# Kernel optimization log

Measured on AMD Instinct MI355X. Metric: run time of the kernel, lower is better.

## Reference

```python
import jax, jax.numpy as jnp
import numpy as np

B, Q, K = 4, 512, 512
QUERY_SIZE = 512
KEY_SIZE = 512
NUM_HIDDENS = 256


def setup_inputs() -> dict:
    key = jax.random.key(0)
    k1, k2, k3, k4, k5 = jax.random.split(key, 5)
    queries = jax.random.normal(k1, (B, Q, 1, QUERY_SIZE), dtype=jnp.float32)
    keys = jax.random.normal(k2, (B, 1, K, KEY_SIZE), dtype=jnp.float32)
    # nn.Linear weights (bias=False); stored as (in, out) for einsum clarity
    W_q = jax.random.normal(k3, (QUERY_SIZE, NUM_HIDDENS), dtype=jnp.float32) * (1.0 / np.sqrt(QUERY_SIZE))
    W_k = jax.random.normal(k4, (KEY_SIZE, NUM_HIDDENS), dtype=jnp.float32) * (1.0 / np.sqrt(KEY_SIZE))
    w_v = jax.random.normal(k5, (NUM_HIDDENS,), dtype=jnp.float32) * (1.0 / np.sqrt(NUM_HIDDENS))
    return {"queries": queries, "keys": keys, "W_q": W_q, "W_k": W_k, "w_v": w_v}


def reference(queries, keys, W_q, W_k, w_v):
    # Project: queries (B,Q,1,Dq) -> (B,Q,1,H); keys (B,1,K,Dk) -> (B,1,K,H)
    q = jnp.einsum('bqod,dh->bqoh', queries, W_q)
    k = jnp.einsum('bokd,dh->bokh', keys, W_k)
    # Broadcast add -> (B,Q,K,H), tanh, reduce hidden via w_v -> (B,Q,K)
    features = jnp.tanh(q + k)
    scores = jnp.einsum('bqkh,h->bqk', features, w_v)
    return scores
```

## Files before the change

kernel.cpp:

```cpp
#include <hip/hip_runtime.h>
#include <hip/hip_bf16.h>

#define HH 256
#define DD 512
#define MM 2048
#define CSCALE 2.8853900817779268f

typedef __bf16 bf16x8 __attribute__((ext_vector_type(8)));
typedef float floatx4 __attribute__((ext_vector_type(4)));

__global__ __launch_bounds__(256) void prep_kernel(
    const float* __restrict__ Wq, const float* __restrict__ Wk,
    const float* __restrict__ wv,
    const float* __restrict__ queries, const float* __restrict__ keys,
    __bf16* __restrict__ Wt, __bf16* __restrict__ Xbf,
    float* __restrict__ wv2, float* __restrict__ sumWp)
{
  const int bx = blockIdx.x;
  if (bx < 256) {
    const int mat  = bx >> 7;
    const int tile = bx & 127;
    const int kt = tile & 15;
    const int nt = tile >> 4;
    const float* __restrict__ W = mat ? Wk : Wq;
    __bf16* __restrict__ Wo = Wt + (size_t)mat * HH * DD;
    __shared__ float lds[32][33];
    const int i = threadIdx.x >> 5;
    const int j = threadIdx.x & 31;
    const int k0 = kt * 32, n0 = nt * 32;
#pragma unroll
    for (int p = 0; p < 4; ++p)
      lds[i + p * 8][j] = W[(k0 + i + p * 8) * HH + n0 + j];
    __syncthreads();
#pragma unroll
    for (int p = 0; p < 4; ++p) {
      const int n = i + p * 8;
      Wo[(n0 + n) * DD + k0 + j] = (__bf16)(lds[j][n] * CSCALE);
    }
  } else if (bx == 256) {
    __shared__ float red[256];
    const int t = threadIdx.x;
    float w = wv[t];
    wv2[t] = -2.0f * w;
    red[t] = w;
    __syncthreads();
    for (int s = 128; s > 0; s >>= 1) {
      if (t < s) red[t] += red[t + s];
      __syncthreads();
    }
    if (t == 0) *sumWp = red[0];
  } else {
    const int blk = bx - 257;
    const size_t dst = (size_t)blk * 2048 + threadIdx.x * 8;
    const float* __restrict__ src =
        (blk < 512) ? (queries + dst) : (keys + dst - (size_t)1048576);
    float4 a = *(const float4*)(src);
    float4 b = *(const float4*)(src + 4);
    bf16x8 v;
    v[0] = (__bf16)a.x; v[1] = (__bf16)a.y; v[2] = (__bf16)a.z; v[3] = (__bf16)a.w;
    v[4] = (__bf16)b.x; v[5] = (__bf16)b.y; v[6] = (__bf16)b.z; v[7] = (__bf16)b.w;
    *(bf16x8*)(Xbf + dst) = v;
  }
}

__global__ __launch_bounds__(256, 4) void proj_kernel(
    const __bf16* __restrict__ Xbf, const __bf16* __restrict__ Wt,
    float* __restrict__ eqp, __bf16* __restrict__ ekb)
{
  const int w    = threadIdx.x >> 6;
  const int lane = threadIdx.x & 63;
  const int quad = lane >> 4;
  const int r    = lane & 15;
  const int tw = w & 1;
  const int ks = w >> 1;
  const bool is_k = (blockIdx.z != 0);
  const __bf16* __restrict__ X  = Xbf + (is_k ? (size_t)1048576 : 0);
  const __bf16* __restrict__ Wb = Wt + (is_k ? (size_t)HH * DD : 0);

  const int m0 = blockIdx.x * 32 + tw * 16;
  const int n0 = blockIdx.y * 32;

  floatx4 acc0 = {0.f, 0.f, 0.f, 0.f};
  floatx4 acc1 = {0.f, 0.f, 0.f, 0.f};
  const __bf16* arow = X + (size_t)(m0 + r) * DD + ks * 256 + quad * 8;
  const __bf16* b0   = Wb + (size_t)(n0 + r) * DD + ks * 256 + quad * 8;
  const __bf16* b1   = b0 + 16 * DD;

#pragma unroll
  for (int kk = 0; kk < 256; kk += 32) {
    bf16x8 af  = *(const bf16x8*)(arow + kk);
    bf16x8 bf0 = *(const bf16x8*)(b0 + kk);
    bf16x8 bf1 = *(const bf16x8*)(b1 + kk);
    acc0 = __builtin_amdgcn_mfma_f32_16x16x32_bf16(af, bf0, acc0, 0, 0, 0);
    acc1 = __builtin_amdgcn_mfma_f32_16x16x32_bf16(af, bf1, acc1, 0, 0, 0);
  }

  __shared__ float part[2][64][9];
  if (ks == 1) {
#pragma unroll
    for (int i = 0; i < 4; ++i) {
      part[tw][lane][i]     = acc0[i];
      part[tw][lane][4 + i] = acc1[i];
    }
  }
  __syncthreads();
  if (ks == 0) {
#pragma unroll
    for (int i = 0; i < 4; ++i) {
      acc0[i] += part[tw][lane][i];
      acc1[i] += part[tw][lane][4 + i];
    }
    const int mrow = m0 + quad * 4;
    if (!is_k) {
#pragma unroll
      for (int i = 0; i < 4; ++i) {
        eqp[(size_t)(mrow + i) * HH + n0 + r] =
            __builtin_amdgcn_exp2f(acc0[i]);
        eqp[(size_t)(mrow + i) * HH + n0 + 16 + r] =
            __builtin_amdgcn_exp2f(acc1[i]);
      }
    } else {
      const int na = n0 + r, nb = n0 + 16 + r;
#pragma unroll
      for (int i = 0; i < 4; ++i) {
        const int m = mrow + i;
        ekb[(((size_t)(m >> 4) * 64 + (na >> 2)) * 16 + (m & 15)) * 4 + (na & 3)] =
            (__bf16)__builtin_amdgcn_exp2f(acc0[i]);
        ekb[(((size_t)(m >> 4) * 64 + (nb >> 2)) * 16 + (m & 15)) * 4 + (nb & 3)] =
            (__bf16)__builtin_amdgcn_exp2f(acc1[i]);
      }
    }
  }
}

__device__ __forceinline__ float quad_term(
    float ek0, float ek1, float ek2, float ek3,
    float4 e, float4 w, float acc)
{
  float u0 = fmaf(e.x, ek0, 1.0f);
  float u1 = fmaf(e.y, ek1, 1.0f);
  float u2 = fmaf(e.z, ek2, 1.0f);
  float u3 = fmaf(e.w, ek3, 1.0f);
  float p01 = u0 * u1;
  float p23 = u2 * u3;
  float n01 = fmaf(w.y, u0, w.x * u1);
  float n23 = fmaf(w.w, u2, w.z * u3);
  float N   = fmaf(n23, p01, n01 * p23);
  float r   = __builtin_amdgcn_rcpf(p01 * p23);
  return fmaf(N, r, acc);
}

__global__ __launch_bounds__(512, 8) void score_kernel(
    const float* __restrict__ eqp, const uint2* __restrict__ ekb,
    const float* __restrict__ wv2, const float* __restrict__ sumWp,
    float* __restrict__ out)
{
  __shared__ __align__(16) float eqs[2][4][128];
  __shared__ __align__(16) float wvs[2][128];
  __shared__ __align__(16) float part[4][256];

  const int tid = threadIdx.x;
  const int t   = tid & 255;
  const int hb  = tid >> 8;
  const int b   = blockIdx.z;
  const int k   = blockIdx.x * 256 + t;
  const int q0  = blockIdx.y * 4;

  {
    const int i0 = tid, i1 = tid + 512;
    eqs[0][(i0 >> 7) & 3][i0 & 127] =
        eqp[(size_t)(b * 512 + q0 + ((i0 >> 7) & 3)) * HH + (i0 & 127)];
    eqs[1][(i1 >> 7) & 3][i1 & 127] =
        eqp[(size_t)(b * 512 + q0 + ((i1 >> 7) & 3)) * HH + 128 + (i1 & 127)];
    if (tid < 256) wvs[tid >> 7][tid & 127] = wv2[tid];
  }
  __syncthreads();

  const int m = b * 512 + k;
  const uint2* __restrict__ kptr =
      ekb + ((size_t)(m >> 4) * 64 + hb * 32) * 16 + (m & 15);

  float acc0 = 0.f, acc1 = 0.f, acc2 = 0.f, acc3 = 0.f;

  for (int c = 0; c < 8; ++c) {
    uint2 kb[4];
#pragma unroll
    for (int i = 0; i < 4; ++i)
      kb[i] = kptr[(c * 4 + i) * 16];
#pragma unroll
    for (int i = 0; i < 4; ++i) {
      const int hq = c * 4 + i;
      float ek0 = __uint_as_float(kb[i].x << 16);
      float ek1 = __uint_as_float(kb[i].x & 0xffff0000u);
      float ek2 = __uint_as_float(kb[i].y << 16);
      float ek3 = __uint_as_float(kb[i].y & 0xffff0000u);
      float4 w4 = *(const float4*)&wvs[hb][hq * 4];
      acc0 = quad_term(ek0, ek1, ek2, ek3, *(const float4*)&eqs[hb][0][hq * 4], w4, acc0);
      acc1 = quad_term(ek0, ek1, ek2, ek3, *(const float4*)&eqs[hb][1][hq * 4], w4, acc1);
      acc2 = quad_term(ek0, ek1, ek2, ek3, *(const float4*)&eqs[hb][2][hq * 4], w4, acc2);
      acc3 = quad_term(ek0, ek1, ek2, ek3, *(const float4*)&eqs[hb][3][hq * 4], w4, acc3);
    }
  }

  if (hb == 1) {
    part[0][t] = acc0; part[1][t] = acc1;
    part[2][t] = acc2; part[3][t] = acc3;
  }
  __syncthreads();
  if (hb == 0) {
    const float sumW = *sumWp;
    float* obase = out + ((size_t)(b * 512 + q0)) * 512 + blockIdx.x * 256 + t;
    obase[0]    = sumW + acc0 + part[0][t];
    obase[512]  = sumW + acc1 + part[1][t];
    obase[1024] = sumW + acc2 + part[2][t];
    obase[1536] = sumW + acc3 + part[3][t];
  }
}

extern "C" void kernel_launch(void* const* d_in, const int* in_sizes, int n_in,
                              void* d_out, int out_size, void* d_ws, size_t ws_size,
                              hipStream_t stream) {
  (void)in_sizes; (void)n_in; (void)out_size; (void)ws_size;
  const float* queries = (const float*)d_in[0];
  const float* Keys    = (const float*)d_in[1];
  const float* Wq      = (const float*)d_in[2];
  const float* Wk      = (const float*)d_in[3];
  const float* wv      = (const float*)d_in[4];
  float* out = (float*)d_out;

  char* ws = (char*)d_ws;
  __bf16* Wt    = (__bf16*)ws;
  float*  wv2   = (float*)(ws + (512 << 10));
  float*  sumWp = (float*)(ws + (513 << 10));
  __bf16* Xbf   = (__bf16*)(ws + (1 << 20));
  float*  eqp   = (float*)(ws + (5ull << 20));
  __bf16* ekb   = (__bf16*)(ws + (7ull << 20));

  prep_kernel<<<dim3(1281), 256, 0, stream>>>(
      Wq, Wk, wv, queries, Keys, Wt, Xbf, wv2, sumWp);
  proj_kernel<<<dim3(64, 8, 2), 256, 0, stream>>>(Xbf, Wt, eqp, ekb);
  score_kernel<<<dim3(2, 128, 4), 512, 0, stream>>>(
      eqp, (const uint2*)ekb, wv2, sumWp, out);
}
```

Measured before the change: 107.4 us.

## Vectorize score math with packed FP32 pairs over two queries

The score inner loop now works on two-wide float vectors, so packed FP32 FMA/mul instructions can process two query rows per operation. To feed this, the key exponentials are stored as duplicated fp32 pairs instead of bf16, and the query and weight tiles in LDS are transposed or duplicated into pair-friendly layouts. The aim is to halve VALU instruction count in the compute-bound score loop. In exchange, key-side global traffic rises roughly fourfold (bf16 to duplicated fp32) and the workspace footprint grows, and the reciprocals stay scalar.

```diff
diff --git a/kernel.cpp b/kernel.cpp
--- a/kernel.cpp
+++ b/kernel.cpp
@@ -8,6 +8,7 @@
 
 typedef __bf16 bf16x8 __attribute__((ext_vector_type(8)));
 typedef float floatx4 __attribute__((ext_vector_type(4)));
+typedef float float2v __attribute__((ext_vector_type(2)));
 
 __global__ __launch_bounds__(256) void prep_kernel(
     const float* __restrict__ Wq, const float* __restrict__ Wk,
@@ -65,7 +66,7 @@
 
 __global__ __launch_bounds__(256, 4) void proj_kernel(
     const __bf16* __restrict__ Xbf, const __bf16* __restrict__ Wt,
-    float* __restrict__ eqp, __bf16* __restrict__ ekb)
+    float* __restrict__ eqp, float2* __restrict__ ekd)
 {
   const int w    = threadIdx.x >> 6;
   const int lane = threadIdx.x & 63;
@@ -124,40 +125,52 @@
 #pragma unroll
       for (int i = 0; i < 4; ++i) {
         const int m = mrow + i;
-        ekb[(((size_t)(m >> 4) * 64 + (na >> 2)) * 16 + (m & 15)) * 4 + (na & 3)] =
-            (__bf16)__builtin_amdgcn_exp2f(acc0[i]);
-        ekb[(((size_t)(m >> 4) * 64 + (nb >> 2)) * 16 + (m & 15)) * 4 + (nb & 3)] =
-            (__bf16)__builtin_amdgcn_exp2f(acc1[i]);
+        float va = __builtin_amdgcn_exp2f(acc0[i]);
+        float vb = __builtin_amdgcn_exp2f(acc1[i]);
+        ekd[(((size_t)(m >> 4) * 64 + (na >> 2)) * 16 + (m & 15)) * 4 + (na & 3)] =
+            make_float2(va, va);
+        ekd[(((size_t)(m >> 4) * 64 + (nb >> 2)) * 16 + (m & 15)) * 4 + (nb & 3)] =
+            make_float2(vb, vb);
       }
     }
   }
 }
 
-__device__ __forceinline__ float quad_term(
-    float ek0, float ek1, float ek2, float ek3,
-    float4 e, float4 w, float acc)
-{
-  float u0 = fmaf(e.x, ek0, 1.0f);
-  float u1 = fmaf(e.y, ek1, 1.0f);
-  float u2 = fmaf(e.z, ek2, 1.0f);
-  float u3 = fmaf(e.w, ek3, 1.0f);
-  float p01 = u0 * u1;
-  float p23 = u2 * u3;
-  float n01 = fmaf(w.y, u0, w.x * u1);
-  float n23 = fmaf(w.w, u2, w.z * u3);
-  float N   = fmaf(n23, p01, n01 * p23);
-  float r   = __builtin_amdgcn_rcpf(p01 * p23);
-  return fmaf(N, r, acc);
+__device__ __forceinline__ float2v pkfma(float2v a, float2v b, float2v c) {
+  return __builtin_elementwise_fma(a, b, c);
+}
+__device__ __forceinline__ float2v lo2(float4 v) { return (float2v){v.x, v.y}; }
+__device__ __forceinline__ float2v hi2(float4 v) { return (float2v){v.z, v.w}; }
+
+__device__ __forceinline__ float2v quad_pair(
+    float2v e0, float2v e1, float2v e2, float2v e3,
+    float2v k0, float2v k1, float2v k2, float2v k3,
+    float2v w0, float2v w1, float2v w2, float2v w3,
+    float2v acc)
+{
+  const float2v one = {1.0f, 1.0f};
+  float2v U0 = pkfma(e0, k0, one);
+  float2v U1 = pkfma(e1, k1, one);
+  float2v U2 = pkfma(e2, k2, one);
+  float2v U3 = pkfma(e3, k3, one);
+  float2v P01 = U0 * U1;
+  float2v P23 = U2 * U3;
+  float2v N01 = pkfma(U0, w1, U1 * w0);
+  float2v N23 = pkfma(U2, w3, U3 * w2);
+  float2v N   = pkfma(N23, P01, N01 * P23);
+  float2v D   = P01 * P23;
+  float2v R   = {__builtin_amdgcn_rcpf(D.x), __builtin_amdgcn_rcpf(D.y)};
+  return pkfma(N, R, acc);
 }
 
 __global__ __launch_bounds__(512, 8) void score_kernel(
-    const float* __restrict__ eqp, const uint2* __restrict__ ekb,
+    const float* __restrict__ eqp, const float4* __restrict__ ekd,
     const float* __restrict__ wv2, const float* __restrict__ sumWp,
     float* __restrict__ out)
 {
-  __shared__ __align__(16) float eqs[2][4][128];
-  __shared__ __align__(16) float wvs[2][128];
-  __shared__ __align__(16) float part[4][256];
+  __shared__ __align__(16) float  eqt[2][128][4];
+  __shared__ __align__(16) float2 wvd[2][128];
+  __shared__ __align__(16) float  part[4][256];
 
   const int tid = threadIdx.x;
   const int t   = tid & 255;
@@ -167,53 +180,65 @@
   const int q0  = blockIdx.y * 4;
 
   {
-    const int i0 = tid, i1 = tid + 512;
-    eqs[0][(i0 >> 7) & 3][i0 & 127] =
-        eqp[(size_t)(b * 512 + q0 + ((i0 >> 7) & 3)) * HH + (i0 & 127)];
-    eqs[1][(i1 >> 7) & 3][i1 & 127] =
-        eqp[(size_t)(b * 512 + q0 + ((i1 >> 7) & 3)) * HH + 128 + (i1 & 127)];
-    if (tid < 256) wvs[tid >> 7][tid & 127] = wv2[tid];
+    const int c = tid & 255;
+    const int r0 = tid >> 8;
+    const int r1 = r0 + 2;
+    float v0 = eqp[(size_t)(b * 512 + q0 + r0) * HH + c];
+    float v1 = eqp[(size_t)(b * 512 + q0 + r1) * HH + c];
+    eqt[c >> 7][c & 127][r0] = v0;
+    eqt[c >> 7][c & 127][r1] = v1;
+    if (tid < 256) {
+      float w = wv2[tid];
+      wvd[tid >> 7][tid & 127] = make_float2(w, w);
+    }
   }
   __syncthreads();
 
   const int m = b * 512 + k;
-  const uint2* __restrict__ kptr =
-      ekb + ((size_t)(m >> 4) * 64 + hb * 32) * 16 + (m & 15);
-
-  float acc0 = 0.f, acc1 = 0.f, acc2 = 0.f, acc3 = 0.f;
-
-  for (int c = 0; c < 8; ++c) {
-    uint2 kb[4];
-#pragma unroll
-    for (int i = 0; i < 4; ++i)
-      kb[i] = kptr[(c * 4 + i) * 16];
-#pragma unroll
-    for (int i = 0; i < 4; ++i) {
-      const int hq = c * 4 + i;
-      float ek0 = __uint_as_float(kb[i].x << 16);
-      float ek1 = __uint_as_float(kb[i].x & 0xffff0000u);
-      float ek2 = __uint_as_float(kb[i].y << 16);
-      float ek3 = __uint_as_float(kb[i].y & 0xffff0000u);
-      float4 w4 = *(const float4*)&wvs[hb][hq * 4];
-      acc0 = quad_term(ek0, ek1, ek2, ek3, *(const float4*)&eqs[hb][0][hq * 4], w4, acc0);
-      acc1 = quad_term(ek0, ek1, ek2, ek3, *(const float4*)&eqs[hb][1][hq * 4], w4, acc1);
-      acc2 = quad_term(ek0, ek1, ek2, ek3, *(const float4*)&eqs[hb][2][hq * 4], w4, acc2);
-      acc3 = quad_term(ek0, ek1, ek2, ek3, *(const float4*)&eqs[hb][3][hq * 4], w4, acc3);
+  const float4* __restrict__ kbase =
+      ekd + ((size_t)(m >> 4) * 64 + hb * 32) * 32 + (m & 15) * 2;
+
+  float2v accA01 = {0.f, 0.f}, accA23 = {0.f, 0.f};
+
+  for (int c = 0; c < 16; ++c) {
+    float4 kl[2][2];
+#pragma unroll
+    for (int i = 0; i < 2; ++i) {
+      kl[i][0] = kbase[(c * 2 + i) * 32];
+      kl[i][1] = kbase[(c * 2 + i) * 32 + 1];
+    }
+#pragma unroll
+    for (int i = 0; i < 2; ++i) {
+      const int hq = (c * 2 + i) & 31;
+      float4 e0 = *(const float4*)&eqt[hb][hq * 4 + 0][0];
+      float4 e1 = *(const float4*)&eqt[hb][hq * 4 + 1][0];
+      float4 e2 = *(const float4*)&eqt[hb][hq * 4 + 2][0];
+      float4 e3 = *(const float4*)&eqt[hb][hq * 4 + 3][0];
+      float4 wA = *(const float4*)&wvd[hb][hq * 4 + 0];
+      float4 wB = *(const float4*)&wvd[hb][hq * 4 + 2];
+      float2v k0 = lo2(kl[i][0]), k1 = hi2(kl[i][0]);
+      float2v k2 = lo2(kl[i][1]), k3 = hi2(kl[i][1]);
+      accA01 = quad_pair(lo2(e0), lo2(e1), lo2(e2), lo2(e3),
+                         k0, k1, k2, k3,
+                         lo2(wA), hi2(wA), lo2(wB), hi2(wB), accA01);
+      accA23 = quad_pair(hi2(e0), hi2(e1), hi2(e2), hi2(e3),
+                         k0, k1, k2, k3,
+                         lo2(wA), hi2(wA), lo2(wB), hi2(wB), accA23);
     }
   }
 
   if (hb == 1) {
-    part[0][t] = acc0; part[1][t] = acc1;
-    part[2][t] = acc2; part[3][t] = acc3;
+    part[0][t] = accA01.x; part[1][t] = accA01.y;
+    part[2][t] = accA23.x; part[3][t] = accA23.y;
   }
   __syncthreads();
   if (hb == 0) {
     const float sumW = *sumWp;
     float* obase = out + ((size_t)(b * 512 + q0)) * 512 + blockIdx.x * 256 + t;
-    obase[0]    = sumW + acc0 + part[0][t];
-    obase[512]  = sumW + acc1 + part[1][t];
-    obase[1024] = sumW + acc2 + part[2][t];
-    obase[1536] = sumW + acc3 + part[3][t];
+    obase[0]    = sumW + accA01.x + part[0][t];
+    obase[512]  = sumW + accA01.y + part[1][t];
+    obase[1024] = sumW + accA23.x + part[2][t];
+    obase[1536] = sumW + accA23.y + part[3][t];
   }
 }
 
@@ -234,11 +259,11 @@
   float*  sumWp = (float*)(ws + (513 << 10));
   __bf16* Xbf   = (__bf16*)(ws + (1 << 20));
   float*  eqp   = (float*)(ws + (5ull << 20));
-  __bf16* ekb   = (__bf16*)(ws + (7ull << 20));
+  float2* ekd   = (float2*)(ws + (7ull << 20));
 
   prep_kernel<<<dim3(1281), 256, 0, stream>>>(
       Wq, Wk, wv, queries, Keys, Wt, Xbf, wv2, sumWp);
-  proj_kernel<<<dim3(64, 8, 2), 256, 0, stream>>>(Xbf, Wt, eqp, ekb);
+  proj_kernel<<<dim3(64, 8, 2), 256, 0, stream>>>(Xbf, Wt, eqp, ekd);
   score_kernel<<<dim3(2, 128, 4), 512, 0, stream>>>(
-      eqp, (const uint2*)ekb, wv2, sumWp, out);
-}
+      eqp, (const float4*)ekd, wv2, sumWp, out);
+}
```

New measurement: 115.9 us. 1.08x slower.

## Fuse input bf16 conversion into projection and store query exponentials as bf16

Applied to the files above, without the earlier changes.

Drops the separate pass that converts queries and keys to bf16. The projection kernel now reads fp32 inputs directly and converts them in registers, which saves a write and re-read of an intermediate buffer. Query exp values are stored as bf16 instead of fp32, halving that buffer and the score kernel's shared-memory footprint. The score loop is restructured to use wide LDS loads and unpack bf16 values. In exchange, the projection kernel reads fp32 inputs eight times (once per n-tile) rather than bf16, and query precision drops.

```diff
diff --git a/kernel.cpp b/kernel.cpp
--- a/kernel.cpp
+++ b/kernel.cpp
@@ -12,9 +12,7 @@
 __global__ __launch_bounds__(256) void prep_kernel(
     const float* __restrict__ Wq, const float* __restrict__ Wk,
     const float* __restrict__ wv,
-    const float* __restrict__ queries, const float* __restrict__ keys,
-    __bf16* __restrict__ Wt, __bf16* __restrict__ Xbf,
-    float* __restrict__ wv2, float* __restrict__ sumWp)
+    __bf16* __restrict__ Wt, float* __restrict__ wv2, float* __restrict__ sumWp)
 {
   const int bx = blockIdx.x;
   if (bx < 256) {
@@ -37,7 +35,7 @@
       const int n = i + p * 8;
       Wo[(n0 + n) * DD + k0 + j] = (__bf16)(lds[j][n] * CSCALE);
     }
-  } else if (bx == 256) {
+  } else {
     __shared__ float red[256];
     const int t = threadIdx.x;
     float w = wv[t];
@@ -49,23 +47,13 @@
       __syncthreads();
     }
     if (t == 0) *sumWp = red[0];
-  } else {
-    const int blk = bx - 257;
-    const size_t dst = (size_t)blk * 2048 + threadIdx.x * 8;
-    const float* __restrict__ src =
-        (blk < 512) ? (queries + dst) : (keys + dst - (size_t)1048576);
-    float4 a = *(const float4*)(src);
-    float4 b = *(const float4*)(src + 4);
-    bf16x8 v;
-    v[0] = (__bf16)a.x; v[1] = (__bf16)a.y; v[2] = (__bf16)a.z; v[3] = (__bf16)a.w;
-    v[4] = (__bf16)b.x; v[5] = (__bf16)b.y; v[6] = (__bf16)b.z; v[7] = (__bf16)b.w;
-    *(bf16x8*)(Xbf + dst) = v;
   }
 }
 
 __global__ __launch_bounds__(256, 4) void proj_kernel(
-    const __bf16* __restrict__ Xbf, const __bf16* __restrict__ Wt,
-    float* __restrict__ eqp, __bf16* __restrict__ ekb)
+    const float* __restrict__ queries, const float* __restrict__ keys,
+    const __bf16* __restrict__ Wt,
+    __bf16* __restrict__ eqb, __bf16* __restrict__ ekb)
 {
   const int w    = threadIdx.x >> 6;
   const int lane = threadIdx.x & 63;
@@ -74,7 +62,7 @@
   const int tw = w & 1;
   const int ks = w >> 1;
   const bool is_k = (blockIdx.z != 0);
-  const __bf16* __restrict__ X  = Xbf + (is_k ? (size_t)1048576 : 0);
+  const float* __restrict__ X  = is_k ? keys : queries;
   const __bf16* __restrict__ Wb = Wt + (is_k ? (size_t)HH * DD : 0);
 
   const int m0 = blockIdx.x * 32 + tw * 16;
@@ -82,13 +70,19 @@
 
   floatx4 acc0 = {0.f, 0.f, 0.f, 0.f};
   floatx4 acc1 = {0.f, 0.f, 0.f, 0.f};
-  const __bf16* arow = X + (size_t)(m0 + r) * DD + ks * 256 + quad * 8;
+  const float*  arow = X + (size_t)(m0 + r) * DD + ks * 256 + quad * 8;
   const __bf16* b0   = Wb + (size_t)(n0 + r) * DD + ks * 256 + quad * 8;
   const __bf16* b1   = b0 + 16 * DD;
 
 #pragma unroll
   for (int kk = 0; kk < 256; kk += 32) {
-    bf16x8 af  = *(const bf16x8*)(arow + kk);
+    float4 a0 = *(const float4*)(arow + kk);
+    float4 a1 = *(const float4*)(arow + kk + 4);
+    bf16x8 af;
+    af[0] = (__bf16)a0.x; af[1] = (__bf16)a0.y;
+    af[2] = (__bf16)a0.z; af[3] = (__bf16)a0.w;
+    af[4] = (__bf16)a1.x; af[5] = (__bf16)a1.y;
+    af[6] = (__bf16)a1.z; af[7] = (__bf16)a1.w;
     bf16x8 bf0 = *(const bf16x8*)(b0 + kk);
     bf16x8 bf1 = *(const bf16x8*)(b1 + kk);
     acc0 = __builtin_amdgcn_mfma_f32_16x16x32_bf16(af, bf0, acc0, 0, 0, 0);
@@ -114,10 +108,10 @@
     if (!is_k) {
 #pragma unroll
       for (int i = 0; i < 4; ++i) {
-        eqp[(size_t)(mrow + i) * HH + n0 + r] =
-            __builtin_amdgcn_exp2f(acc0[i]);
-        eqp[(size_t)(mrow + i) * HH + n0 + 16 + r] =
-            __builtin_amdgcn_exp2f(acc1[i]);
+        eqb[(size_t)(mrow + i) * HH + n0 + r] =
+            (__bf16)__builtin_amdgcn_exp2f(acc0[i]);
+        eqb[(size_t)(mrow + i) * HH + n0 + 16 + r] =
+            (__bf16)__builtin_amdgcn_exp2f(acc1[i]);
       }
     } else {
       const int na = n0 + r, nb = n0 + 16 + r;
@@ -133,14 +127,22 @@
   }
 }
 
+__device__ __forceinline__ float bf_lo(unsigned u) {
+  return __uint_as_float(u << 16);
+}
+__device__ __forceinline__ float bf_hi(unsigned u) {
+  return __uint_as_float(u & 0xffff0000u);
+}
+
 __device__ __forceinline__ float quad_term(
     float ek0, float ek1, float ek2, float ek3,
-    float4 e, float4 w, float acc)
-{
-  float u0 = fmaf(e.x, ek0, 1.0f);
-  float u1 = fmaf(e.y, ek1, 1.0f);
-  float u2 = fmaf(e.z, ek2, 1.0f);
-  float u3 = fmaf(e.w, ek3, 1.0f);
+    float e0, float e1, float e2, float e3,
+    float4 w, float acc)
+{
+  float u0 = fmaf(e0, ek0, 1.0f);
+  float u1 = fmaf(e1, ek1, 1.0f);
+  float u2 = fmaf(e2, ek2, 1.0f);
+  float u3 = fmaf(e3, ek3, 1.0f);
   float p01 = u0 * u1;
   float p23 = u2 * u3;
   float n01 = fmaf(w.y, u0, w.x * u1);
@@ -151,11 +153,11 @@
 }
 
 __global__ __launch_bounds__(512, 8) void score_kernel(
-    const float* __restrict__ eqp, const uint2* __restrict__ ekb,
+    const __bf16* __restrict__ eqb, const uint2* __restrict__ ekb,
     const float* __restrict__ wv2, const float* __restrict__ sumWp,
     float* __restrict__ out)
 {
-  __shared__ __align__(16) float eqs[2][4][128];
+  __shared__ __align__(16) unsigned eqsu[2][4][64];
   __shared__ __align__(16) float wvs[2][128];
   __shared__ __align__(16) float part[4][256];
 
@@ -167,11 +169,11 @@
   const int q0  = blockIdx.y * 4;
 
   {
-    const int i0 = tid, i1 = tid + 512;
-    eqs[0][(i0 >> 7) & 3][i0 & 127] =
-        eqp[(size_t)(b * 512 + q0 + ((i0 >> 7) & 3)) * HH + (i0 & 127)];
-    eqs[1][(i1 >> 7) & 3][i1 & 127] =
-        eqp[(size_t)(b * 512 + q0 + ((i1 >> 7) & 3)) * HH + 128 + (i1 & 127)];
+    const int q = tid >> 7;
+    const int p = tid & 127;
+    const unsigned* __restrict__ qrow =
+        (const unsigned*)(eqb + (size_t)(b * 512 + q0 + q) * HH);
+    eqsu[p >> 6][q][p & 63] = qrow[p];
     if (tid < 256) wvs[tid >> 7][tid & 127] = wv2[tid];
   }
   __syncthreads();
@@ -182,23 +184,39 @@
 
   float acc0 = 0.f, acc1 = 0.f, acc2 = 0.f, acc3 = 0.f;
 
-  for (int c = 0; c < 8; ++c) {
-    uint2 kb[4];
-#pragma unroll
-    for (int i = 0; i < 4; ++i)
-      kb[i] = kptr[(c * 4 + i) * 16];
-#pragma unroll
-    for (int i = 0; i < 4; ++i) {
-      const int hq = c * 4 + i;
-      float ek0 = __uint_as_float(kb[i].x << 16);
-      float ek1 = __uint_as_float(kb[i].x & 0xffff0000u);
-      float ek2 = __uint_as_float(kb[i].y << 16);
-      float ek3 = __uint_as_float(kb[i].y & 0xffff0000u);
-      float4 w4 = *(const float4*)&wvs[hb][hq * 4];
-      acc0 = quad_term(ek0, ek1, ek2, ek3, *(const float4*)&eqs[hb][0][hq * 4], w4, acc0);
-      acc1 = quad_term(ek0, ek1, ek2, ek3, *(const float4*)&eqs[hb][1][hq * 4], w4, acc1);
-      acc2 = quad_term(ek0, ek1, ek2, ek3, *(const float4*)&eqs[hb][2][hq * 4], w4, acc2);
-      acc3 = quad_term(ek0, ek1, ek2, ek3, *(const float4*)&eqs[hb][3][hq * 4], w4, acc3);
+#pragma unroll 1
+  for (int c = 0; c < 16; ++c) {
+    uint2 ka = kptr[(c * 2 + 0) * 16];
+    uint2 kc = kptr[(c * 2 + 1) * 16];
+    uint4 r0 = *(const uint4*)&eqsu[hb][0][c * 4];
+    uint4 r1 = *(const uint4*)&eqsu[hb][1][c * 4];
+    uint4 r2 = *(const uint4*)&eqsu[hb][2][c * 4];
+    uint4 r3 = *(const uint4*)&eqsu[hb][3][c * 4];
+    float4 wa = *(const float4*)&wvs[hb][c * 8];
+    float4 wb = *(const float4*)&wvs[hb][c * 8 + 4];
+    {
+      float p0 = bf_lo(ka.x), p1 = bf_hi(ka.x);
+      float p2 = bf_lo(ka.y), p3 = bf_hi(ka.y);
+      acc0 = quad_term(p0, p1, p2, p3,
+                       bf_lo(r0.x), bf_hi(r0.x), bf_lo(r0.y), bf_hi(r0.y), wa, acc0);
+      acc1 = quad_term(p0, p1, p2, p3,
+                       bf_lo(r1.x), bf_hi(r1.x), bf_lo(r1.y), bf_hi(r1.y), wa, acc1);
+      acc2 = quad_term(p0, p1, p2, p3,
+                       bf_lo(r2.x), bf_hi(r2.x), bf_lo(r2.y), bf_hi(r2.y), wa, acc2);
+      acc3 = quad_term(p0, p1, p2, p3,
+                       bf_lo(r3.x), bf_hi(r3.x), bf_lo(r3.y), bf_hi(r3.y), wa, acc3);
+    }
+    {
+      float p0 = bf_lo(kc.x), p1 = bf_hi(kc.x);
+      float p2 = bf_lo(kc.y), p3 = bf_hi(kc.y);
+      acc0 = quad_term(p0, p1, p2, p3,
+                       bf_lo(r0.z), bf_hi(r0.z), bf_lo(r0.w), bf_hi(r0.w), wb, acc0);
+      acc1 = quad_term(p0, p1, p2, p3,
+                       bf_lo(r1.z), bf_hi(r1.z), bf_lo(r1.w), bf_hi(r1.w), wb, acc1);
+      acc2 = quad_term(p0, p1, p2, p3,
+                       bf_lo(r2.z), bf_hi(r2.z), bf_lo(r2.w), bf_hi(r2.w), wb, acc2);
+      acc3 = quad_term(p0, p1, p2, p3,
+                       bf_lo(r3.z), bf_hi(r3.z), bf_lo(r3.w), bf_hi(r3.w), wb, acc3);
     }
   }
 
@@ -232,13 +250,11 @@
   __bf16* Wt    = (__bf16*)ws;
   float*  wv2   = (float*)(ws + (512 << 10));
   float*  sumWp = (float*)(ws + (513 << 10));
-  __bf16* Xbf   = (__bf16*)(ws + (1 << 20));
-  float*  eqp   = (float*)(ws + (5ull << 20));
-  __bf16* ekb   = (__bf16*)(ws + (7ull << 20));
-
-  prep_kernel<<<dim3(1281), 256, 0, stream>>>(
-      Wq, Wk, wv, queries, Keys, Wt, Xbf, wv2, sumWp);
-  proj_kernel<<<dim3(64, 8, 2), 256, 0, stream>>>(Xbf, Wt, eqp, ekb);
+  __bf16* eqb   = (__bf16*)(ws + (1 << 20));
+  __bf16* ekb   = (__bf16*)(ws + (2 << 20));
+
+  prep_kernel<<<dim3(257), 256, 0, stream>>>(Wq, Wk, wv, Wt, wv2, sumWp);
+  proj_kernel<<<dim3(64, 8, 2), 256, 0, stream>>>(queries, Keys, Wt, eqb, ekb);
   score_kernel<<<dim3(2, 128, 4), 512, 0, stream>>>(
-      eqp, (const uint2*)ekb, wv2, sumWp, out);
-}
+      eqb, (const uint2*)ekb, wv2, sumWp, out);
+}
```

New measurement: 113.0 us. +5.2%, slower.
